# Kernel optimization log

Hardware: AMD Instinct MI355X
Metric: run time of the kernel (lower is better)

The kernel has to match this reference:

```python
import jax, jax.numpy as jnp
import numpy as np
import math

N, E, C, NB, NEL, NG = 8192, 131072, 64, 8, 4, 16
R_MAX, AVG_NEI, P_CUT, NL, SH = 5.0, 16.0, 6, 2, 16


def _sph(u):
    # real spherical harmonics l=0..3, component normalization (sum_m Y_lm^2 = 2l+1 on unit sphere)
    x, y, z = u[:, 0], u[:, 1], u[:, 2]
    s3, s15, s5 = math.sqrt(3.0), math.sqrt(15.0), math.sqrt(5.0)
    s105, s7 = math.sqrt(105.0), math.sqrt(7.0)
    c35, c21 = math.sqrt(35.0 / 8.0), math.sqrt(21.0 / 8.0)
    Y = [jnp.ones_like(x),
         s3 * x, s3 * y, s3 * z,
         s15 * x * y, s15 * y * z, 0.5 * s5 * (3 * z * z - 1), s15 * x * z, 0.5 * s15 * (x * x - y * y),
         c35 * y * (3 * x * x - y * y), s105 * x * y * z, c21 * y * (5 * z * z - 1),
         0.5 * s7 * (5 * z ** 3 - 3 * z), c21 * x * (5 * z * z - 1),
         0.5 * s105 * z * (x * x - y * y), c35 * x * (x * x - 3 * y * y)]
    return jnp.stack(Y, axis=-1)  # [E,16]


def _bessel(r):
    k = jnp.arange(1, NB + 1, dtype=r.dtype)
    return math.sqrt(2.0 / R_MAX) * jnp.sin(k * jnp.pi * r[:, None] / R_MAX) / r[:, None]


def _poly_cutoff(r):
    p = float(P_CUT)
    x = r / R_MAX
    f = (1.0 - 0.5 * (p + 1) * (p + 2) * x ** p + p * (p + 2) * x ** (p + 1)
         - 0.5 * p * (p + 1) * x ** (p + 2))
    return f * (x < 1.0)


def setup_inputs() -> dict:
    key = jax.random.key(0)
    ks = jax.random.split(key, 16)
    sc = lambda fan: 1.0 / math.sqrt(fan)
    return {
        "pos": 2.0 * jax.random.normal(ks[0], (N, 3), jnp.float32),
        "atom_types": jax.random.randint(ks[1], (N,), 0, NEL),
        "edge_index": jax.random.randint(ks[2], (2, E), 0, N),
        "batch": jnp.sort(jax.random.randint(ks[3], (N,), 0, NG)),
        "W_embed": jax.random.normal(ks[4], (NEL, C), jnp.float32),
        "W_r1": sc(NB) * jax.random.normal(ks[5], (NL, NB, 64), jnp.float32),
        "W_r2": sc(64) * jax.random.normal(ks[6], (NL, 64, 64), jnp.float32),
        "W_r3": sc(64) * jax.random.normal(ks[7], (NL, 64, C), jnp.float32),
        "W_sc": sc(C) * jax.random.normal(ks[8], (NL, NEL, C, C), jnp.float32),
        "w_prod": 0.5 * jax.random.normal(ks[9], (NL, NEL, 4), jnp.float32),
        "w_ro0": sc(C) * jax.random.normal(ks[10], (C,), jnp.float32),
        "W_ro1a": sc(C) * jax.random.normal(ks[11], (C, 16), jnp.float32),
        "w_ro1b": sc(16) * jax.random.normal(ks[12], (16,), jnp.float32),
    }


def reference(pos, atom_types, edge_index, batch, W_embed, W_r1, W_r2, W_r3,
              W_sc, w_prod, w_ro0, W_ro1a, w_ro1b):
    src, dst = edge_index[0], edge_index[1]
    vec = pos[dst] - pos[src]                      # [E,3]
    r = jnp.sqrt(jnp.sum(vec * vec, -1) + 1e-12)   # [E]
    Y = _sph(vec / r[:, None])                     # [E,SH]
    edge_feats = _bessel(r) * _poly_cutoff(r)[:, None]  # [E,NB]
    h = W_embed[atom_types]                        # one-hot @ W == lookup, [N,C]
    energies = [jnp.zeros((NG,), pos.dtype)]       # pair_repulsion disabled
    for i in range(NL):
        Rw = jax.nn.silu(edge_feats @ W_r1[i])
        Rw = jax.nn.silu(Rw @ W_r2[i])
        Rw = Rw @ W_r3[i]                          # radial MLP weights [E,C]
        # gather-TP-scatter: message [E,C,SH] -> node A [N,C,SH]
        m = (Rw * h[src])[:, :, None] * Y[:, None, :]
        A = jax.ops.segment_sum(m.reshape(E, C * SH), dst,
                                num_segments=N).reshape(N, C, SH) / AVG_NEI
        sc_feat = jnp.einsum('nc,ncd->nd', h, W_sc[i][atom_types])  # element-dep skip
        inv = jnp.stack([A[:, :, 0],
                         jnp.sum(A[:, :, 1:4] ** 2, -1),
                         jnp.sum(A[:, :, 4:9] ** 2, -1),
                         jnp.sum(A[:, :, 9:16] ** 2, -1)], axis=-1)  # [N,C,4]
        h = jnp.einsum('ncj,nj->nc', inv, w_prod[i][atom_types]) + sc_feat
        if i < NL - 1:
            e_node = h @ w_ro0                     # linear readout
        else:
            e_node = jax.nn.silu(h @ W_ro1a) @ w_ro1b  # gated MLP readout
        energies.append(jax.ops.segment_sum(e_node, batch, num_segments=NG))
    contributions = jnp.stack(energies, -1)        # [NG, NL+1]
    return jnp.sum(contributions, -1)              # total energy per graph
```

## Files before the change

kernel.cpp:

```cpp
#include <hip/hip_runtime.h>
#include <hip/hip_bf16.h>
#include <math.h>

#define N_NODES 8192
#define N_EDGES 131072
#define NGRP 16
#define NLAY 2
#define NELM 4
constexpr float INV_AVG = 1.0f / 16.0f;
constexpr float PI_F = 3.14159265358979323846f;

#define CV_POS   0
#define CV_EMB   24576
#define CV_SC    42240
#define CV_PROD  75008
#define CV_RO0   75040
#define CV_RO1A  75104
#define CV_RO1B  76128
#define CVT_N    76144

#define SWZ_PER_L 10240
#define SWZ_N     20480

#define B_CVT  230
#define B_SWZ  80
#define B_HIST 512
#define CVT_WORK 58736

typedef __hip_bfloat16 bf16;
typedef __attribute__((ext_vector_type(8))) short bf16x8;
typedef __attribute__((ext_vector_type(4))) float f32x4;

__device__ __forceinline__ float silu_f(float x){ return x / (1.0f + __expf(-x)); }
__device__ __forceinline__ float bfbits2f(unsigned short u){
  return __uint_as_float(((unsigned)u) << 16);
}
__device__ __forceinline__ void unpack2(unsigned u, float& lo, float& hi){
  lo = __uint_as_float(u << 16);
  hi = __uint_as_float(u & 0xffff0000u);
}
__device__ __forceinline__ short f2bs(float v){
  union { bf16 b; short s; } u; u.b = __float2bfloat16(v); return u.s;
}
__device__ __forceinline__ float ldf(const void* p, int i, int flag){
  if (flag) return bfbits2f(((const unsigned short*)p)[i]);
  return ((const float*)p)[i];
}
__device__ __forceinline__ int detect_fl(const void* pos){
  int lane = threadIdx.x & 63;
  const unsigned short* u = (const unsigned short*)pos;
  float va = bfbits2f(u[2*lane]), vb = bfbits2f(u[2*lane+1]);
  bool bad = !(fabsf(va) <= 1000.0f) || !(fabsf(vb) <= 1000.0f);
  return (__ballot(bad) == 0ull) ? 1 : 0;
}
__device__ __forceinline__ void WSYNC(){ __builtin_amdgcn_wave_barrier(); }

__device__ __forceinline__ void gl_lds4(const void* g, void* l){
  __builtin_amdgcn_global_load_lds(
      (const __attribute__((address_space(1))) unsigned*)g,
      (__attribute__((address_space(3))) unsigned*)l, 4, 0, 0);
}

__global__ void k_setup1(const void* __restrict__ pos, const void* __restrict__ Wemb,
                         const void* __restrict__ Wsc, const void* __restrict__ wprod,
                         const void* __restrict__ wro0, const void* __restrict__ Wro1a,
                         const void* __restrict__ wro1b, const void* __restrict__ Wr1,
                         const void* __restrict__ Wr2, const void* __restrict__ Wr3,
                         const int* __restrict__ dstp, float* __restrict__ cv,
                         short* __restrict__ swz, int* __restrict__ deg){
  int b = blockIdx.x, tix = threadIdx.x;
  if (b >= B_CVT + B_SWZ){
    int e = (b - B_CVT - B_SWZ)*256 + tix;
    atomicAdd(&deg[dstp[e]], 1);
    return;
  }
  int fl = detect_fl(pos);
  if (b < B_CVT){
    int i = b*256 + tix;
    if (i < 24576){ cv[CV_POS + i] = ldf(pos, i, fl); return; }
    if (i < 24832){ int j=i-24576; cv[CV_EMB + j] = ldf(Wemb, j, fl); return; }
    if (i < 57600){ int j=i-24832; cv[CV_SC  + j] = ldf(Wsc,  j, fl); return; }
    if (i < 57632){ int j=i-57600; cv[CV_PROD+ j] = ldf(wprod,j, fl); return; }
    if (i < 57696){ int j=i-57632; cv[CV_RO0 + j] = ldf(wro0, j, fl); return; }
    if (i < 58720){ int j=i-57696; cv[CV_RO1A+ j] = ldf(Wro1a,j, fl); return; }
    if (i < CVT_WORK){ int j=i-58720; cv[CV_RO1B+ j] = ldf(wro1b,j, fl); return; }
    return;
  }
  int i = (b - B_CVT)*256 + tix;
  int l = i / SWZ_PER_L, w = i % SWZ_PER_L;
  float v;
  if (w < 2048){
    int t = w >> 9, q = (w >> 7) & 3, n = (w >> 3) & 15, j = w & 7;
    int k = q*8 + j;
    v = (k < 8) ? ldf(Wr1, l*512 + k*64 + t*16 + n, fl) : 0.0f;
  } else if (w < 6144){
    int w2 = w - 2048;
    int nt = w2 >> 10, kt = (w2 >> 9) & 1, q = (w2 >> 7) & 3, n = (w2 >> 3) & 15, j = w2 & 7;
    int k = kt*32 + q*8 + j;
    v = ldf(Wr2, l*4096 + k*64 + nt*16 + n, fl);
  } else {
    int w3 = w - 6144;
    int nt = w3 >> 10, kt = (w3 >> 9) & 1, q = (w3 >> 7) & 3, n = (w3 >> 3) & 15, j = w3 & 7;
    int k = kt*32 + q*8 + j;
    v = ldf(Wr3, l*4096 + k*64 + nt*16 + n, fl);
  }
  swz[i] = f2bs(v);
}

__global__ void k_scan(const int* __restrict__ deg, int* __restrict__ row_start,
                       int* __restrict__ cursor, float* __restrict__ ene2){
  __shared__ int lds[1024];
  int t = threadIdx.x;
  if (t < 8*NGRP) ene2[t] = 0.0f;
  int v[8]; int tot = 0;
#pragma unroll
  for (int k = 0; k < 8; k++){ v[k] = deg[t*8+k]; tot += v[k]; }
  lds[t] = tot; __syncthreads();
  for (int off = 1; off < 1024; off <<= 1){
    int x = (t >= off) ? lds[t-off] : 0;
    __syncthreads();
    lds[t] += x;
    __syncthreads();
  }
  int base = lds[t] - tot;
#pragma unroll
  for (int k = 0; k < 8; k++){ row_start[t*8+k] = base; cursor[t*8+k] = base; base += v[k]; }
  if (t == 1023) row_start[N_NODES] = base;
}

__global__ void k_fillgeom(const int* __restrict__ ei, int* __restrict__ cursor,
                           const float* __restrict__ posf, const int* __restrict__ types,
                           int* __restrict__ sslot, unsigned char* __restrict__ tsl,
                           unsigned short* __restrict__ Yb, float* __restrict__ rbuf){
  int e = blockIdx.x*256 + threadIdx.x;
  int s = ei[e], d = ei[N_EDGES + e];
  int slot = atomicAdd(&cursor[d], 1);
  sslot[slot] = s;
  tsl[slot] = (unsigned char)types[s];
  float vx = posf[d*3+0] - posf[s*3+0];
  float vy = posf[d*3+1] - posf[s*3+1];
  float vz = posf[d*3+2] - posf[s*3+2];
  float r = sqrtf(vx*vx + vy*vy + vz*vz + 1e-12f);
  float ir = 1.0f / r;
  float x = vx*ir, y = vy*ir, z = vz*ir;
  const float s3 = 1.7320508075688772f, s15 = 3.872983346207417f, s5 = 2.23606797749979f;
  const float s105 = 10.246950765959598f, s7 = 2.6457513110645907f;
  const float c35 = 2.091650066335189f, c21 = 1.6201851746019651f;
  float x2 = x*x, y2 = y*y, z2 = z*z;
  float ys[16] = {
    1.0f, s3*x, s3*y, s3*z,
    s15*x*y, s15*y*z, 0.5f*s5*(3.0f*z2-1.0f), s15*x*z,
    0.5f*s15*(x2-y2), c35*y*(3.0f*x2-y2), s105*x*y*z, c21*y*(5.0f*z2-1.0f),
    0.5f*s7*(5.0f*z2*z-3.0f*z), c21*x*(5.0f*z2-1.0f), 0.5f*s105*z*(x2-y2),
    c35*x*(x2-3.0f*y2) };
  union { bf16 b[16]; uint4 u[2]; } pk;
#pragma unroll
  for (int k = 0; k < 16; k++) pk.b[k] = __float2bfloat16(ys[k]);
  uint4* yp = (uint4*)(Yb + (size_t)slot*16);
  yp[0] = pk.u[0];
  yp[1] = pk.u[1];
  rbuf[slot] = r;
}

#define ROWS 72
template<int LAYER_KIND>
__global__ void __launch_bounds__(64) k_gu(const short* __restrict__ sw,
        const float* __restrict__ rbuf, const unsigned char* __restrict__ tsl,
        const int* __restrict__ sslot, const float* __restrict__ h_old,
        float* __restrict__ h_new, const unsigned short* __restrict__ Yb,
        const int* __restrict__ row_start, const int* __restrict__ types,
        const float* __restrict__ Wsc, const float* __restrict__ wprod,
        const float* __restrict__ wemb, const float* __restrict__ wro0,
        const float* __restrict__ Wro1a, const float* __restrict__ wro1b,
        const int* __restrict__ batch, float* __restrict__ ene2){
  __shared__ __align__(16) short A_[16*ROWS];
  __shared__ __align__(16) float hS[LAYER_KIND ? 16 : 1][64];
  __shared__ __align__(16) unsigned short yS[16][16];
  __shared__ float hn_l[64];
  int lane = threadIdx.x;
  int q = lane >> 4, nn = lane & 15;
  int n = blockIdx.x;
  int beg = row_start[n], end = row_start[n + 1];
  short* A = A_;

  const bf16x8* S1 = (const bf16x8*)(sw);
  const bf16x8* S2 = (const bf16x8*)(sw + 2048);
  const bf16x8* S3 = (const bf16x8*)(sw + 6144);

  float e0=0.f, e1=0.f, e2=0.f, e3=0.f;
  if (LAYER_KIND == 0){
    e0 = wemb[lane]; e1 = wemb[64+lane]; e2 = wemb[128+lane]; e3 = wemb[192+lane];
  }

  float acc[16];
#pragma unroll
  for (int s = 0; s < 16; s++) acc[s] = 0.0f;

  for (int cb = beg; cb < end; cb += 16){
    int cnt = min(16, end - cb);
    WSYNC();
    const char* ysrc = (const char*)Yb + (size_t)cb*32 + lane*4;
    gl_lds4(ysrc,       &yS[0][0]);
    gl_lds4(ysrc + 256, &yS[8][0]);
    int tv = 0;
    if (LAYER_KIND == 0){
      tv = (int)tsl[min(cb + nn, N_EDGES - 1)];
    } else {
      int sv = sslot[min(cb + nn, N_EDGES - 1)];
      for (int i = 0; i < cnt; i++){
        int src = __builtin_amdgcn_readlane(sv, i);
        gl_lds4(h_old + (size_t)src*64 + lane, &hS[i][0]);
      }
    }
    {
      float r = rbuf[min(cb + nn, N_EDGES - 1)];
      float xc = r * 0.2f;
      float f = 0.0f;
      if (xc < 1.0f){
        float x3 = xc*xc*xc, x6 = x3*x3, x7 = x6*xc, x8 = x7*xc;
        f = 1.0f - 28.0f*x6 + 48.0f*x7 - 21.0f*x8;
      }
      float bs = 0.6324555320336759f * f / r;
      float t0 = PI_F * r * 0.2f;
      bf16x8 af1 = {0,0,0,0,0,0,0,0};
      if (q == 0){
#pragma unroll
        for (int j = 0; j < 8; j++) af1[j] = f2bs(bs * __sinf((float)(j+1) * t0));
      }
      f32x4 macc[4];
#pragma unroll
      for (int t = 0; t < 4; t++){
        bf16x8 b = S1[t*64 + q*16 + nn];
        f32x4 z = {0.f,0.f,0.f,0.f};
        macc[t] = __builtin_amdgcn_mfma_f32_16x16x32_bf16(af1, b, z, 0, 0, 0);
      }
#pragma unroll
      for (int t = 0; t < 4; t++)
#pragma unroll
        for (int rg = 0; rg < 4; rg++)
          A[(q*4+rg)*ROWS + t*16 + nn] = f2bs(silu_f(macc[t][rg]));
      WSYNC();
      bf16x8 a0 = *(const bf16x8*)&A[nn*ROWS + 0*32 + q*8];
      bf16x8 a1 = *(const bf16x8*)&A[nn*ROWS + 1*32 + q*8];
      WSYNC();
#pragma unroll
      for (int t = 0; t < 4; t++){
        f32x4 z = {0.f,0.f,0.f,0.f};
        bf16x8 b0 = S2[t*128 + 0*64 + q*16 + nn];
        bf16x8 b1 = S2[t*128 + 1*64 + q*16 + nn];
        z = __builtin_amdgcn_mfma_f32_16x16x32_bf16(a0, b0, z, 0, 0, 0);
        z = __builtin_amdgcn_mfma_f32_16x16x32_bf16(a1, b1, z, 0, 0, 0);
        macc[t] = z;
      }
#pragma unroll
      for (int t = 0; t < 4; t++)
#pragma unroll
        for (int rg = 0; rg < 4; rg++)
          A[(q*4+rg)*ROWS + t*16 + nn] = f2bs(silu_f(macc[t][rg]));
      WSYNC();
      a0 = *(const bf16x8*)&A[nn*ROWS + 0*32 + q*8];
      a1 = *(const bf16x8*)&A[nn*ROWS + 1*32 + q*8];
      WSYNC();
#pragma unroll
      for (int t = 0; t < 4; t++){
        f32x4 z = {0.f,0.f,0.f,0.f};
        bf16x8 b0 = S3[t*128 + 0*64 + q*16 + nn];
        bf16x8 b1 = S3[t*128 + 1*64 + q*16 + nn];
        z = __builtin_amdgcn_mfma_f32_16x16x32_bf16(a0, b0, z, 0, 0, 0);
        z = __builtin_amdgcn_mfma_f32_16x16x32_bf16(a1, b1, z, 0, 0, 0);
        macc[t] = z;
      }
#pragma unroll
      for (int t = 0; t < 4; t++)
#pragma unroll
        for (int rg = 0; rg < 4; rg++)
          A[(q*4+rg)*ROWS + t*16 + nn] = f2bs(macc[t][rg]);
      WSYNC();
    }
    asm volatile("s_waitcnt vmcnt(0)" ::: "memory");
    __builtin_amdgcn_sched_barrier(0);
    for (int i = 0; i < cnt; i++){
      float rw = bfbits2f((unsigned short)A[i*ROWS + lane]);
      float hv;
      if (LAYER_KIND == 0){
        int ty = __builtin_amdgcn_readlane(tv, i);
        hv = (ty & 2) ? ((ty & 1) ? e3 : e2) : ((ty & 1) ? e1 : e0);
      } else {
        hv = hS[i][lane];
      }
      float g = rw * hv;
      const uint4* yq = (const uint4*)&yS[i][0];
      uint4 ya = yq[0], yb = yq[1];
      float lo, hi;
      unpack2(ya.x, lo, hi); acc[0]  += g*lo; acc[1]  += g*hi;
      unpack2(ya.y, lo, hi); acc[2]  += g*lo; acc[3]  += g*hi;
      unpack2(ya.z, lo, hi); acc[4]  += g*lo; acc[5]  += g*hi;
      unpack2(ya.w, lo, hi); acc[6]  += g*lo; acc[7]  += g*hi;
      unpack2(yb.x, lo, hi); acc[8]  += g*lo; acc[9]  += g*hi;
      unpack2(yb.y, lo, hi); acc[10] += g*lo; acc[11] += g*hi;
      unpack2(yb.z, lo, hi); acc[12] += g*lo; acc[13] += g*hi;
      unpack2(yb.w, lo, hi); acc[14] += g*lo; acc[15] += g*hi;
    }
  }
#pragma unroll
  for (int s = 0; s < 16; s++) acc[s] *= INV_AVG;

  int ty = __builtin_amdgcn_readfirstlane(types[n]);
  const float* Ws = Wsc + (size_t)ty*4096;
  const float* hrow = (LAYER_KIND == 0) ? (wemb + ty*64) : (h_old + (size_t)n*64);
  float sc0 = 0.f, sc1 = 0.f, sc2 = 0.f, sc3 = 0.f;
#pragma unroll
  for (int c = 0; c < 64; c += 4){
    sc0 += hrow[c+0] * Ws[(c+0)*64 + lane];
    sc1 += hrow[c+1] * Ws[(c+1)*64 + lane];
    sc2 += hrow[c+2] * Ws[(c+2)*64 + lane];
    sc3 += hrow[c+3] * Ws[(c+3)*64 + lane];
  }
  float sc = (sc0 + sc1) + (sc2 + sc3);

  float inv0 = acc[0];
  float inv1 = acc[1]*acc[1] + acc[2]*acc[2] + acc[3]*acc[3];
  float inv2 = acc[4]*acc[4] + acc[5]*acc[5] + acc[6]*acc[6] + acc[7]*acc[7]
             + acc[8]*acc[8];
  float inv3 = acc[9]*acc[9] + acc[10]*acc[10] + acc[11]*acc[11] + acc[12]*acc[12]
             + acc[13]*acc[13] + acc[14]*acc[14] + acc[15]*acc[15];
  const float* wp = wprod + ty*4;
  float hn = inv0*wp[0] + inv1*wp[1] + inv2*wp[2] + inv3*wp[3] + sc;
  if (LAYER_KIND == 0)
    h_new[(size_t)n*64 + lane] = hn;

  float ev;
  if (LAYER_KIND == 0){
    float p = hn * wro0[lane];
#pragma unroll
    for (int off = 32; off >= 1; off >>= 1) p += __shfl_xor(p, off, 64);
    ev = p;
  } else {
    hn_l[lane] = hn;
    WSYNC();
    int j = lane & 15;
    float pj = 0.0f;
#pragma unroll
    for (int c = 0; c < 64; c++)
      pj += hn_l[c] * Wro1a[c*16 + j];
    float evj = silu_f(pj) * wro1b[j];
    evj += __shfl_xor(evj, 8, 64);
    evj += __shfl_xor(evj, 4, 64);
    evj += __shfl_xor(evj, 2, 64);
    evj += __shfl_xor(evj, 1, 64);
    ev = evj;
  }
  if (lane == 0) atomicAdd(&ene2[(n & 7)*NGRP + batch[n]], ev);
}

__global__ void k_out(const float* __restrict__ ene2, const void* __restrict__ pos,
                      void* __restrict__ out){
  int fl = detect_fl(pos);
  int t = threadIdx.x;
  if (t < NGRP){
    float v = 0.0f;
#pragma unroll
    for (int k = 0; k < 8; k++) v += ene2[k*NGRP + t];
    if (fl) ((bf16*)out)[t] = __float2bfloat16(v);
    else    ((float*)out)[t] = v;
  }
}

static inline size_t rup(size_t x){ return (x + 255) & ~(size_t)255; }

extern "C" void kernel_launch(void* const* d_in, const int* in_sizes, int n_in,
                              void* d_out, int out_size, void* d_ws, size_t ws_size,
                              hipStream_t stream) {
  const void* pos   = d_in[0];
  const int*  types = (const int*)d_in[1];
  const int*  ei    = (const int*)d_in[2];
  const int*  batch = (const int*)d_in[3];
  const void* Wemb  = d_in[4];
  const void* Wr1   = d_in[5];
  const void* Wr2   = d_in[6];
  const void* Wr3   = d_in[7];
  const void* Wsc   = d_in[8];
  const void* wprod = d_in[9];
  const void* wro0  = d_in[10];
  const void* Wro1a = d_in[11];
  const void* wro1b = d_in[12];

  char* w = (char*)d_ws;
  float* cv       = (float*)w; w += rup((size_t)CVT_N*4);
  short* swz      = (short*)w; w += rup((size_t)SWZ_N*2);
  float* ene2     = (float*)w; w += 512;
  int*   deg      = (int*)  w; w += rup((size_t)N_NODES*4);
  int*   row_start= (int*)  w; w += rup((size_t)(N_NODES+1)*4);
  int*   cursor   = (int*)  w; w += rup((size_t)N_NODES*4);
  int*   sslot    = (int*)  w; w += rup((size_t)N_EDGES*4);
  unsigned char* tsl = (unsigned char*)w; w += rup((size_t)N_EDGES);
  float* hbuf     = (float*)w; w += rup((size_t)N_NODES*64*4);
  float* rbuf     = (float*)w; w += rup((size_t)N_EDGES*4);
  unsigned short* Yb = (unsigned short*)w; w += rup((size_t)N_EDGES*16*2);
  w += 4096;

  hipMemsetAsync(deg, 0, N_NODES*4, stream);

  const int* dstp = ei + N_EDGES;
  k_setup1<<<B_CVT + B_SWZ + B_HIST, 256, 0, stream>>>(
      pos, Wemb, Wsc, wprod, wro0, Wro1a, wro1b, Wr1, Wr2, Wr3, dstp, cv, swz, deg);
  k_scan<<<1, 1024, 0, stream>>>(deg, row_start, cursor, ene2);
  k_fillgeom<<<N_EDGES/256, 256, 0, stream>>>(ei, cursor, cv + CV_POS, types,
      sslot, tsl, Yb, rbuf);

  k_gu<0><<<N_NODES, 64, 0, stream>>>(swz, rbuf, tsl, sslot,
      hbuf , hbuf , Yb, row_start, types,
      cv + CV_SC, cv + CV_PROD, cv + CV_EMB,
      cv + CV_RO0, cv + CV_RO1A, cv + CV_RO1B, batch, ene2);
  k_gu<1><<<N_NODES, 64, 0, stream>>>(swz + SWZ_PER_L, rbuf, tsl, sslot,
      hbuf , hbuf , Yb, row_start, types,
      cv + CV_SC + (size_t)NELM*4096, cv + CV_PROD + NELM*4, cv + CV_EMB,
      cv + CV_RO0, cv + CV_RO1A, cv + CV_RO1B, batch, ene2);

  k_out<<<1, 64, 0, stream>>>(ene2, pos, d_out);
}
```

Measured before the change: 188.1 us.

## Replace CSR scan with fixed-stride per-node slots and fuse setup kernels

Drops the degree histogram, the single-block prefix scan and the separate geometry fill. Each destination node now gets a fixed 64-slot bucket filled by atomic cursor, so geometry, weight conversion and swizzling all run in one setup kernel, removing two launches and a serial scan. Layer 0's skip term is precomputed per element type, since the layer-0 input depends only on atom type. The trade-off is that edge buffers grow 4x with sparse, strided rows, and any node with more than 64 incoming edges would overflow its bucket and corrupt the next one.

Measured after the change: 176.2 us. 1.07x faster.

```diff
diff --git a/kernel.cpp b/kernel.cpp
--- a/kernel.cpp
+++ b/kernel.cpp
@@ -7,25 +7,28 @@
 #define NGRP 16
 #define NLAY 2
 #define NELM 4
+#define SLOT_STRIDE 64
+#define N_SLOTS (N_NODES*SLOT_STRIDE)
 constexpr float INV_AVG = 1.0f / 16.0f;
 constexpr float PI_F = 3.14159265358979323846f;
 
-#define CV_POS   0
-#define CV_EMB   24576
-#define CV_SC    42240
-#define CV_PROD  75008
-#define CV_RO0   75040
-#define CV_RO1A  75104
-#define CV_RO1B  76128
-#define CVT_N    76144
+#define CV_EMB   0
+#define CV_SC    256
+#define CV_PROD  33024
+#define CV_RO0   33056
+#define CV_RO1A  33120
+#define CV_RO1B  34144
+#define CV_SC0T  34160
+#define CVT_WORK 34160
+#define CVT_N    34416
 
 #define SWZ_PER_L 10240
 #define SWZ_N     20480
 
-#define B_CVT  230
+#define B_GEOM 512
+#define B_CVT  134
 #define B_SWZ  80
-#define B_HIST 512
-#define CVT_WORK 58736
+#define SETUP_GRID (B_GEOM + B_CVT + B_SWZ + 1)
 
 typedef __hip_bfloat16 bf16;
 typedef __attribute__((ext_vector_type(8))) short bf16x8;
@@ -61,105 +64,90 @@
       (__attribute__((address_space(3))) unsigned*)l, 4, 0, 0);
 }
 
-__global__ void k_setup1(const void* __restrict__ pos, const void* __restrict__ Wemb,
-                         const void* __restrict__ Wsc, const void* __restrict__ wprod,
-                         const void* __restrict__ wro0, const void* __restrict__ Wro1a,
-                         const void* __restrict__ wro1b, const void* __restrict__ Wr1,
-                         const void* __restrict__ Wr2, const void* __restrict__ Wr3,
-                         const int* __restrict__ dstp, float* __restrict__ cv,
-                         short* __restrict__ swz, int* __restrict__ deg){
+__global__ void k_setup(const void* __restrict__ pos, const int* __restrict__ types,
+                        const int* __restrict__ ei,
+                        const void* __restrict__ Wemb, const void* __restrict__ Wsc,
+                        const void* __restrict__ wprod, const void* __restrict__ wro0,
+                        const void* __restrict__ Wro1a, const void* __restrict__ wro1b,
+                        const void* __restrict__ Wr1, const void* __restrict__ Wr2,
+                        const void* __restrict__ Wr3,
+                        int* __restrict__ cursor, int* __restrict__ sslot,
+                        unsigned char* __restrict__ tsl,
+                        unsigned short* __restrict__ Yb, float* __restrict__ rbuf,
+                        float* __restrict__ cv, short* __restrict__ swz){
   int b = blockIdx.x, tix = threadIdx.x;
-  if (b >= B_CVT + B_SWZ){
-    int e = (b - B_CVT - B_SWZ)*256 + tix;
-    atomicAdd(&deg[dstp[e]], 1);
+  int fl = detect_fl(pos);
+  if (b < B_GEOM){
+    int e = b*256 + tix;
+    int s = ei[e], d = ei[N_EDGES + e];
+    int slot = (d << 6) + atomicAdd(&cursor[d], 1);
+    sslot[slot] = s;
+    tsl[slot] = (unsigned char)types[s];
+    float vx = ldf(pos, d*3+0, fl) - ldf(pos, s*3+0, fl);
+    float vy = ldf(pos, d*3+1, fl) - ldf(pos, s*3+1, fl);
+    float vz = ldf(pos, d*3+2, fl) - ldf(pos, s*3+2, fl);
+    float r = sqrtf(vx*vx + vy*vy + vz*vz + 1e-12f);
+    float ir = 1.0f / r;
+    float x = vx*ir, y = vy*ir, z = vz*ir;
+    const float s3 = 1.7320508075688772f, s15 = 3.872983346207417f, s5 = 2.23606797749979f;
+    const float s105 = 10.246950765959598f, s7 = 2.6457513110645907f;
+    const float c35 = 2.091650066335189f, c21 = 1.6201851746019651f;
+    float x2 = x*x, y2 = y*y, z2 = z*z;
+    float ys[16] = {
+      1.0f, s3*x, s3*y, s3*z,
+      s15*x*y, s15*y*z, 0.5f*s5*(3.0f*z2-1.0f), s15*x*z,
+      0.5f*s15*(x2-y2), c35*y*(3.0f*x2-y2), s105*x*y*z, c21*y*(5.0f*z2-1.0f),
+      0.5f*s7*(5.0f*z2*z-3.0f*z), c21*x*(5.0f*z2-1.0f), 0.5f*s105*z*(x2-y2),
+      c35*x*(x2-3.0f*y2) };
+    union { bf16 bb[16]; uint4 u[2]; } pk;
+#pragma unroll
+    for (int k = 0; k < 16; k++) pk.bb[k] = __float2bfloat16(ys[k]);
+    uint4* yp = (uint4*)(Yb + (size_t)slot*16);
+    yp[0] = pk.u[0];
+    yp[1] = pk.u[1];
+    rbuf[slot] = r;
     return;
   }
-  int fl = detect_fl(pos);
-  if (b < B_CVT){
-    int i = b*256 + tix;
-    if (i < 24576){ cv[CV_POS + i] = ldf(pos, i, fl); return; }
-    if (i < 24832){ int j=i-24576; cv[CV_EMB + j] = ldf(Wemb, j, fl); return; }
-    if (i < 57600){ int j=i-24832; cv[CV_SC  + j] = ldf(Wsc,  j, fl); return; }
-    if (i < 57632){ int j=i-57600; cv[CV_PROD+ j] = ldf(wprod,j, fl); return; }
-    if (i < 57696){ int j=i-57632; cv[CV_RO0 + j] = ldf(wro0, j, fl); return; }
-    if (i < 58720){ int j=i-57696; cv[CV_RO1A+ j] = ldf(Wro1a,j, fl); return; }
-    if (i < CVT_WORK){ int j=i-58720; cv[CV_RO1B+ j] = ldf(wro1b,j, fl); return; }
+  if (b < B_GEOM + B_CVT){
+    int i = (b - B_GEOM)*256 + tix;
+    if (i < 256)  { cv[CV_EMB + i] = ldf(Wemb, i, fl); return; }
+    if (i < 33024){ int j=i-256;   cv[CV_SC  + j] = ldf(Wsc,  j, fl); return; }
+    if (i < 33056){ int j=i-33024; cv[CV_PROD+ j] = ldf(wprod,j, fl); return; }
+    if (i < 33120){ int j=i-33056; cv[CV_RO0 + j] = ldf(wro0, j, fl); return; }
+    if (i < 34144){ int j=i-33120; cv[CV_RO1A+ j] = ldf(Wro1a,j, fl); return; }
+    if (i < CVT_WORK){ int j=i-34144; cv[CV_RO1B+ j] = ldf(wro1b,j, fl); return; }
     return;
   }
-  int i = (b - B_CVT)*256 + tix;
-  int l = i / SWZ_PER_L, w = i % SWZ_PER_L;
-  float v;
-  if (w < 2048){
-    int t = w >> 9, q = (w >> 7) & 3, n = (w >> 3) & 15, j = w & 7;
-    int k = q*8 + j;
-    v = (k < 8) ? ldf(Wr1, l*512 + k*64 + t*16 + n, fl) : 0.0f;
-  } else if (w < 6144){
-    int w2 = w - 2048;
-    int nt = w2 >> 10, kt = (w2 >> 9) & 1, q = (w2 >> 7) & 3, n = (w2 >> 3) & 15, j = w2 & 7;
-    int k = kt*32 + q*8 + j;
-    v = ldf(Wr2, l*4096 + k*64 + nt*16 + n, fl);
-  } else {
-    int w3 = w - 6144;
-    int nt = w3 >> 10, kt = (w3 >> 9) & 1, q = (w3 >> 7) & 3, n = (w3 >> 3) & 15, j = w3 & 7;
-    int k = kt*32 + q*8 + j;
-    v = ldf(Wr3, l*4096 + k*64 + nt*16 + n, fl);
-  }
-  swz[i] = f2bs(v);
-}
-
-__global__ void k_scan(const int* __restrict__ deg, int* __restrict__ row_start,
-                       int* __restrict__ cursor, float* __restrict__ ene2){
-  __shared__ int lds[1024];
-  int t = threadIdx.x;
-  if (t < 8*NGRP) ene2[t] = 0.0f;
-  int v[8]; int tot = 0;
-#pragma unroll
-  for (int k = 0; k < 8; k++){ v[k] = deg[t*8+k]; tot += v[k]; }
-  lds[t] = tot; __syncthreads();
-  for (int off = 1; off < 1024; off <<= 1){
-    int x = (t >= off) ? lds[t-off] : 0;
-    __syncthreads();
-    lds[t] += x;
-    __syncthreads();
-  }
-  int base = lds[t] - tot;
-#pragma unroll
-  for (int k = 0; k < 8; k++){ row_start[t*8+k] = base; cursor[t*8+k] = base; base += v[k]; }
-  if (t == 1023) row_start[N_NODES] = base;
-}
-
-__global__ void k_fillgeom(const int* __restrict__ ei, int* __restrict__ cursor,
-                           const float* __restrict__ posf, const int* __restrict__ types,
-                           int* __restrict__ sslot, unsigned char* __restrict__ tsl,
-                           unsigned short* __restrict__ Yb, float* __restrict__ rbuf){
-  int e = blockIdx.x*256 + threadIdx.x;
-  int s = ei[e], d = ei[N_EDGES + e];
-  int slot = atomicAdd(&cursor[d], 1);
-  sslot[slot] = s;
-  tsl[slot] = (unsigned char)types[s];
-  float vx = posf[d*3+0] - posf[s*3+0];
-  float vy = posf[d*3+1] - posf[s*3+1];
-  float vz = posf[d*3+2] - posf[s*3+2];
-  float r = sqrtf(vx*vx + vy*vy + vz*vz + 1e-12f);
-  float ir = 1.0f / r;
-  float x = vx*ir, y = vy*ir, z = vz*ir;
-  const float s3 = 1.7320508075688772f, s15 = 3.872983346207417f, s5 = 2.23606797749979f;
-  const float s105 = 10.246950765959598f, s7 = 2.6457513110645907f;
-  const float c35 = 2.091650066335189f, c21 = 1.6201851746019651f;
-  float x2 = x*x, y2 = y*y, z2 = z*z;
-  float ys[16] = {
-    1.0f, s3*x, s3*y, s3*z,
-    s15*x*y, s15*y*z, 0.5f*s5*(3.0f*z2-1.0f), s15*x*z,
-    0.5f*s15*(x2-y2), c35*y*(3.0f*x2-y2), s105*x*y*z, c21*y*(5.0f*z2-1.0f),
-    0.5f*s7*(5.0f*z2*z-3.0f*z), c21*x*(5.0f*z2-1.0f), 0.5f*s105*z*(x2-y2),
-    c35*x*(x2-3.0f*y2) };
-  union { bf16 b[16]; uint4 u[2]; } pk;
-#pragma unroll
-  for (int k = 0; k < 16; k++) pk.b[k] = __float2bfloat16(ys[k]);
-  uint4* yp = (uint4*)(Yb + (size_t)slot*16);
-  yp[0] = pk.u[0];
-  yp[1] = pk.u[1];
-  rbuf[slot] = r;
+  if (b < B_GEOM + B_CVT + B_SWZ){
+    int i = (b - B_GEOM - B_CVT)*256 + tix;
+    int l = i / SWZ_PER_L, w = i % SWZ_PER_L;
+    float v;
+    if (w < 2048){
+      int t = w >> 9, q = (w >> 7) & 3, n = (w >> 3) & 15, j = w & 7;
+      int k = q*8 + j;
+      v = (k < 8) ? ldf(Wr1, l*512 + k*64 + t*16 + n, fl) : 0.0f;
+    } else if (w < 6144){
+      int w2 = w - 2048;
+      int nt = w2 >> 10, kt = (w2 >> 9) & 1, q = (w2 >> 7) & 3, n = (w2 >> 3) & 15, j = w2 & 7;
+      int k = kt*32 + q*8 + j;
+      v = ldf(Wr2, l*4096 + k*64 + nt*16 + n, fl);
+    } else {
+      int w3 = w - 6144;
+      int nt = w3 >> 10, kt = (w3 >> 9) & 1, q = (w3 >> 7) & 3, n = (w3 >> 3) & 15, j = w3 & 7;
+      int k = kt*32 + q*8 + j;
+      v = ldf(Wr3, l*4096 + k*64 + nt*16 + n, fl);
+    }
+    swz[i] = f2bs(v);
+    return;
+  }
+  {
+    int ty = tix >> 6, d = tix & 63;
+    float s = 0.0f;
+#pragma unroll 8
+    for (int c = 0; c < 64; c++)
+      s += ldf(Wemb, ty*64 + c, fl) * ldf(Wsc, ty*4096 + c*64 + d, fl);
+    cv[CV_SC0T + tix] = s;
+  }
 }
 
 #define ROWS 72
@@ -168,9 +156,10 @@
         const float* __restrict__ rbuf, const unsigned char* __restrict__ tsl,
         const int* __restrict__ sslot, const float* __restrict__ h_old,
         float* __restrict__ h_new, const unsigned short* __restrict__ Yb,
-        const int* __restrict__ row_start, const int* __restrict__ types,
+        const int* __restrict__ cursor, const int* __restrict__ types,
         const float* __restrict__ Wsc, const float* __restrict__ wprod,
-        const float* __restrict__ wemb, const float* __restrict__ wro0,
+        const float* __restrict__ wemb, const float* __restrict__ sc0t,
+        const float* __restrict__ wro0,
         const float* __restrict__ Wro1a, const float* __restrict__ wro1b,
         const int* __restrict__ batch, float* __restrict__ ene2){
   __shared__ __align__(16) short A_[16*ROWS];
@@ -180,7 +169,8 @@
   int lane = threadIdx.x;
   int q = lane >> 4, nn = lane & 15;
   int n = blockIdx.x;
-  int beg = row_start[n], end = row_start[n + 1];
+  int beg = n << 6;
+  int end = beg + cursor[n];
   short* A = A_;
 
   const bf16x8* S1 = (const bf16x8*)(sw);
@@ -204,16 +194,16 @@
     gl_lds4(ysrc + 256, &yS[8][0]);
     int tv = 0;
     if (LAYER_KIND == 0){
-      tv = (int)tsl[min(cb + nn, N_EDGES - 1)];
+      tv = (int)tsl[cb + nn];
     } else {
-      int sv = sslot[min(cb + nn, N_EDGES - 1)];
+      int sv = sslot[cb + nn];
       for (int i = 0; i < cnt; i++){
         int src = __builtin_amdgcn_readlane(sv, i);
         gl_lds4(h_old + (size_t)src*64 + lane, &hS[i][0]);
       }
     }
     {
-      float r = rbuf[min(cb + nn, N_EDGES - 1)];
+      float r = rbuf[cb + nn];
       float xc = r * 0.2f;
       float f = 0.0f;
       if (xc < 1.0f){
@@ -306,17 +296,22 @@
   for (int s = 0; s < 16; s++) acc[s] *= INV_AVG;
 
   int ty = __builtin_amdgcn_readfirstlane(types[n]);
-  const float* Ws = Wsc + (size_t)ty*4096;
-  const float* hrow = (LAYER_KIND == 0) ? (wemb + ty*64) : (h_old + (size_t)n*64);
-  float sc0 = 0.f, sc1 = 0.f, sc2 = 0.f, sc3 = 0.f;
-#pragma unroll
-  for (int c = 0; c < 64; c += 4){
-    sc0 += hrow[c+0] * Ws[(c+0)*64 + lane];
-    sc1 += hrow[c+1] * Ws[(c+1)*64 + lane];
-    sc2 += hrow[c+2] * Ws[(c+2)*64 + lane];
-    sc3 += hrow[c+3] * Ws[(c+3)*64 + lane];
-  }
-  float sc = (sc0 + sc1) + (sc2 + sc3);
+  float sc;
+  if (LAYER_KIND == 0){
+    sc = sc0t[ty*64 + lane];
+  } else {
+    const float* Ws = Wsc + (size_t)ty*4096;
+    const float* hrow = h_old + (size_t)n*64;
+    float sc0 = 0.f, sc1 = 0.f, sc2 = 0.f, sc3 = 0.f;
+#pragma unroll
+    for (int c = 0; c < 64; c += 4){
+      sc0 += hrow[c+0] * Ws[(c+0)*64 + lane];
+      sc1 += hrow[c+1] * Ws[(c+1)*64 + lane];
+      sc2 += hrow[c+2] * Ws[(c+2)*64 + lane];
+      sc3 += hrow[c+3] * Ws[(c+3)*64 + lane];
+    }
+    sc = (sc0 + sc1) + (sc2 + sc3);
+  }
 
   float inv0 = acc[0];
   float inv1 = acc[1]*acc[1] + acc[2]*acc[2] + acc[3]*acc[3];
@@ -386,36 +381,31 @@
   const void* wro1b = d_in[12];
 
   char* w = (char*)d_ws;
+  float* ene2     = (float*)w; w += 512;
+  int*   cursor   = (int*)  w; w += rup((size_t)N_NODES*4);
   float* cv       = (float*)w; w += rup((size_t)CVT_N*4);
   short* swz      = (short*)w; w += rup((size_t)SWZ_N*2);
-  float* ene2     = (float*)w; w += 512;
-  int*   deg      = (int*)  w; w += rup((size_t)N_NODES*4);
-  int*   row_start= (int*)  w; w += rup((size_t)(N_NODES+1)*4);
-  int*   cursor   = (int*)  w; w += rup((size_t)N_NODES*4);
-  int*   sslot    = (int*)  w; w += rup((size_t)N_EDGES*4);
-  unsigned char* tsl = (unsigned char*)w; w += rup((size_t)N_EDGES);
+  int*   sslot    = (int*)  w; w += rup((size_t)N_SLOTS*4);
+  unsigned char* tsl = (unsigned char*)w; w += rup((size_t)N_SLOTS);
   float* hbuf     = (float*)w; w += rup((size_t)N_NODES*64*4);
-  float* rbuf     = (float*)w; w += rup((size_t)N_EDGES*4);
-  unsigned short* Yb = (unsigned short*)w; w += rup((size_t)N_EDGES*16*2);
+  float* rbuf     = (float*)w; w += rup((size_t)N_SLOTS*4);
+  unsigned short* Yb = (unsigned short*)w; w += rup((size_t)N_SLOTS*16*2);
   w += 4096;
 
-  hipMemsetAsync(deg, 0, N_NODES*4, stream);
-
-  const int* dstp = ei + N_EDGES;
-  k_setup1<<<B_CVT + B_SWZ + B_HIST, 256, 0, stream>>>(
-      pos, Wemb, Wsc, wprod, wro0, Wro1a, wro1b, Wr1, Wr2, Wr3, dstp, cv, swz, deg);
-  k_scan<<<1, 1024, 0, stream>>>(deg, row_start, cursor, ene2);
-  k_fillgeom<<<N_EDGES/256, 256, 0, stream>>>(ei, cursor, cv + CV_POS, types,
-      sslot, tsl, Yb, rbuf);
+  hipMemsetAsync(ene2, 0, 512 + (size_t)N_NODES*4, stream);
+
+  k_setup<<<SETUP_GRID, 256, 0, stream>>>(pos, types, ei,
+      Wemb, Wsc, wprod, wro0, Wro1a, wro1b, Wr1, Wr2, Wr3,
+      cursor, sslot, tsl, Yb, rbuf, cv, swz);
 
   k_gu<0><<<N_NODES, 64, 0, stream>>>(swz, rbuf, tsl, sslot,
-      hbuf , hbuf , Yb, row_start, types,
-      cv + CV_SC, cv + CV_PROD, cv + CV_EMB,
+      hbuf , hbuf , Yb, cursor, types,
+      cv + CV_SC, cv + CV_PROD, cv + CV_EMB, cv + CV_SC0T,
       cv + CV_RO0, cv + CV_RO1A, cv + CV_RO1B, batch, ene2);
   k_gu<1><<<N_NODES, 64, 0, stream>>>(swz + SWZ_PER_L, rbuf, tsl, sslot,
-      hbuf , hbuf , Yb, row_start, types,
+      hbuf , hbuf , Yb, cursor, types,
       cv + CV_SC + (size_t)NELM*4096, cv + CV_PROD + NELM*4, cv + CV_EMB,
-      cv + CV_RO0, cv + CV_RO1A, cv + CV_RO1B, batch, ene2);
+      cv + CV_SC0T, cv + CV_RO0, cv + CV_RO1A, cv + CV_RO1B, batch, ene2);
 
   k_out<<<1, 64, 0, stream>>>(ene2, pos, d_out);
 }
```
